# Kernel optimization log

Hardware: AMD Instinct MI355X
Metric: run time of the kernel (lower is better)

The kernel has to match this reference:

```python
import jax, jax.numpy as jnp
import numpy as np

NA, NW, H = 20000, 100000, 128
DA, DW = 64, 128
E_CR, E_IN, E_CO = 400000, 600000, 300000


def _seg_softmax(logits, seg, n):
    m = jax.ops.segment_max(logits, seg, num_segments=n)
    e = jnp.exp(logits - m[seg])
    s = jax.ops.segment_sum(e, seg, num_segments=n)
    return e / (s[seg] + 1e-16)


def _gat(x_src, x_dst, edge, W, b, a_s, a_d):
    # PyG GATConv, heads=1, concat=False, shared lin for src/dst, add_self_loops=True
    n_src, n_dst = x_src.shape[0], x_dst.shape[0]
    loops = jnp.arange(min(n_src, n_dst), dtype=edge.dtype)
    src = jnp.concatenate([edge[0], loops])
    dst = jnp.concatenate([edge[1], loops])
    hs = x_src @ W            # [n_src, H]
    hd = x_dst @ W            # [n_dst, H]
    logit = jax.nn.leaky_relu((hs @ a_s)[src] + (hd @ a_d)[dst], 0.2)
    alpha = _seg_softmax(logit, dst, n_dst)          # softmax over in-neighborhoods
    out = jax.ops.segment_sum(alpha[:, None] * hs[src], dst, num_segments=n_dst)
    return out + b


def _mlp2(x, w1, b1, w2, b2):
    return jax.nn.relu(x @ w1 + b1) @ w2 + b2


def setup_inputs() -> dict:
    key = jax.random.key(0)
    ks = iter(jax.random.split(key, 40))

    def p(shape, scale=0.1):
        return jax.random.normal(next(ks), shape, jnp.float32) * scale

    def edges(n_src, n_dst, E):
        s = jax.random.randint(next(ks), (E,), 0, n_src, dtype=jnp.int32)
        d = jax.random.randint(next(ks), (E,), 0, n_dst, dtype=jnp.int32)
        d = jnp.where(s == d, (d + 1) % n_dst, d)  # keep input loop-free (PyG strips them)
        return jnp.stack([s, d])

    e_creates = edges(NA, NW, E_CR)
    inp = {
        'artist_feat': jax.random.normal(next(ks), (NA, DA), jnp.float32),
        'work_feat': jax.random.normal(next(ks), (NW, DW), jnp.float32),
        'a_w1': p((DA, H)), 'a_b1': jnp.zeros(H, jnp.float32),
        'a_w2': p((H, H)), 'a_b2': jnp.zeros(H, jnp.float32),
        'w_w1': p((DW, H)), 'w_b1': jnp.zeros(H, jnp.float32),
        'w_w2': p((H, H)), 'w_b2': jnp.zeros(H, jnp.float32),
        'cr_W': p((H, H)), 'cr_b': jnp.zeros(H, jnp.float32), 'cr_as': p((H,)), 'cr_ad': p((H,)),
        'in_W': p((H, H)), 'in_b': jnp.zeros(H, jnp.float32), 'in_as': p((H,)), 'in_ad': p((H,)),
        'co_W': p((H, H)), 'co_b': jnp.zeros(H, jnp.float32), 'co_as': p((H,)), 'co_ad': p((H,)),
        'p_w1': p((2 * H, 256)), 'p_b1': jnp.zeros(256, jnp.float32),
        'p_w2': p((256, 128)), 'p_b2': jnp.zeros(128, jnp.float32),
        'p_w3': p((128, 1)), 'p_b3': jnp.zeros(1, jnp.float32),
        'e_creates': e_creates,
        'e_created_by': jnp.flip(e_creates, axis=0),  # reverse relation [work, artist]
        'e_infl': edges(NW, NW, E_IN),
        'e_collab': edges(NA, NA, E_CO),
    }
    return inp


def reference(artist_feat, work_feat,
              a_w1, a_b1, a_w2, a_b2,
              w_w1, w_b1, w_w2, w_b2,
              cr_W, cr_b, cr_as, cr_ad,
              in_W, in_b, in_as, in_ad,
              co_W, co_b, co_as, co_ad,
              p_w1, p_b1, p_w2, p_b2, p_w3, p_b3,
              e_creates, e_created_by, e_infl, e_collab):
    ax = _mlp2(artist_feat, a_w1, a_b1, a_w2, a_b2)      # [NA, H]
    wx = _mlp2(work_feat, w_w1, w_b1, w_w2, w_b2)        # [NW, H]
    wx = jax.nn.elu(_gat(ax, wx, e_creates, cr_W, cr_b, cr_as, cr_ad))
    wx = jax.nn.elu(_gat(wx, wx, e_infl, in_W, in_b, in_as, in_ad))
    au = _gat(wx, ax, e_created_by, cr_W, cr_b, cr_as, cr_ad)  # no elu (matches source)
    ac = jax.nn.elu(_gat(au, au, e_collab, co_W, co_b, co_as, co_ad))
    comb = jnp.concatenate([au, ac], axis=1)             # [NA, 2H]
    h = jax.nn.relu(comb @ p_w1 + p_b1)                  # dropout is identity in eval
    h = jax.nn.relu(h @ p_w2 + p_b2)
    return (h @ p_w3 + p_b3).squeeze()
```

## Files before the change

### kernel.cpp

```cpp
#include <hip/hip_runtime.h>
#include <hip/hip_bf16.h>
#include <cstddef>

#define NA 20000
#define NW 100000
#define HH 128
#define DA 64
#define E_CR 400000
#define E_IN 600000
#define E_CO 300000

#define ROW1 0
#define ROW2 (NW)
#define ROW3 (2 * NW)
#define ROW4 (2 * NW + NA)
#define NTOT (2 * NW + 2 * NA)
#define CAPW 40
#define CAPA 88
#define GNB ((NA + 127) / 128)
#define NPREPG (7 * 128)

typedef short v8s __attribute__((ext_vector_type(8)));
typedef float v4f __attribute__((ext_vector_type(4)));

constexpr int PSLOT = 2 * 128 * 264;

__device__ inline short f2bf(float x) {
    union { float f; unsigned u; } c; c.f = x;
    unsigned r = c.u + 0x7fff + ((c.u >> 16) & 1);
    return (short)(r >> 16);
}
__device__ inline float bf2f(short s) {
    union { unsigned u; float f; } c; c.u = ((unsigned)(unsigned short)s) << 16;
    return c.f;
}
__device__ inline float bfu2f(unsigned short s) {
    union { unsigned u; float f; } c; c.u = ((unsigned)s) << 16;
    return c.f;
}

__device__ inline void split8(const float* xv, v8s& h, v8s& l) {
#pragma unroll
    for (int p = 0; p < 4; ++p) {
        float2 xf; xf.x = xv[2 * p]; xf.y = xv[2 * p + 1];
        __hip_bfloat162 hb = __float22bfloat162_rn(xf);
        float2 hf = __bfloat1622float2(hb);
        float2 lf; lf.x = xf.x - hf.x; lf.y = xf.y - hf.y;
        __hip_bfloat162 lb = __float22bfloat162_rn(lf);
        union { __hip_bfloat162 b; short2 s; } uh, ul;
        uh.b = hb; ul.b = lb;
        h[2 * p] = uh.s.x; h[2 * p + 1] = uh.s.y;
        l[2 * p] = ul.s.x; l[2 * p + 1] = ul.s.y;
    }
}

struct AppChunk { const int* e; int E; int* pad; int cap; int* deg; };

__device__ inline void do_append(const AppChunk& ap, int bid) {
    int b0 = bid * 1024 + threadIdx.x;
    int s[4], d[4]; bool ok[4];
#pragma unroll
    for (int u = 0; u < 4; ++u) {
        int i = b0 + u * 256;
        ok[u] = i < ap.E;
        s[u] = 0; d[u] = 0;
        if (ok[u]) { s[u] = ap.e[i]; d[u] = ap.e[ap.E + i]; }
    }
    int p[4];
#pragma unroll
    for (int u = 0; u < 4; ++u) if (ok[u]) p[u] = atomicAdd(&ap.deg[d[u]], 1);
#pragma unroll
    for (int u = 0; u < 4; ++u)
        if (ok[u] && p[u] < ap.cap)
            ap.pad[(size_t)d[u] * ap.cap + p[u]] = s[u];
}

struct PrepDesc { const float* src; int ldw; int K; };
struct PrepArgs {
    PrepDesc d[10];
    const float *wvW, *wvA;
    const float *ww2, *aw2, *wb2, *ab2;
    float *uW, *u3, *cons, *bf;
    short* wf;
    const float* gX; const float* gB; float* gY; int gM;
};

__global__ __launch_bounds__(256) void k_prep_append(PrepArgs a, short* __restrict__ out,
        AppChunk ap1, AppChunk ap2, AppChunk ap3, AppChunk ap4)
{
    __shared__ short Bs2[2 * 128 * 72];
    int bx = blockIdx.x;

    if (bx == 0) {
        __shared__ float sv[HH];
        int t = threadIdx.x;
        if (t < HH) {
            float s = 0.f;
            for (int j = 0; j < HH; ++j) s += a.wvW[(size_t)t * HH + j] * a.wvA[j];
            sv[t] = s;
        }
        __syncthreads();
        if (t < HH) {
            float s = 0.f;
            for (int j = 0; j < HH; ++j) s += a.ww2[(size_t)t * HH + j] * sv[j];
            a.uW[t] = s;
        } else {
            int k = t - HH;
            float s = 0.f;
            for (int j = 0; j < HH; ++j) s += a.aw2[(size_t)k * HH + j] * sv[j];
            a.u3[k] = s;
        }
        if (t == 0) {
            float s = 0.f;
            for (int j = 0; j < HH; ++j) s += a.wb2[j] * sv[j];
            a.cons[0] = s;
        }
        if (t == 1) {
            float s = 0.f;
            for (int j = 0; j < HH; ++j) s += a.ab2[j] * sv[j];
            a.cons[1] = s;
        }
        return;
    }
    bx -= 1;
    if (bx < 4) {
        int k = bx * 32 + (threadIdx.x >> 3);
        int cb = (threadIdx.x & 7) * 16;
        for (int c = cb; c < cb + 16; ++c) {
            float s = 0.f;
            for (int j = 0; j < HH; ++j) s += a.aw2[(size_t)k * HH + j] * a.wvW[(size_t)j * HH + c];
            short h = f2bf(s);
            short l = f2bf(s - bf2f(h));
            a.wf[c * 136 + k] = h;
            a.wf[128 * 136 + c * 136 + k] = l;
        }
        if (bx == 0 && threadIdx.x < HH) {
            int c = threadIdx.x;
            float s = 0.f;
            for (int j = 0; j < HH; ++j) s += a.ab2[j] * a.wvW[(size_t)j * HH + c];
            a.bf[c] = s;
        }
        return;
    }
    bx -= 4;
    {
        int n1 = (ap1.E + 1023) >> 10;
        if (bx < n1) { do_append(ap1, bx); return; }
        bx -= n1;
        int n2 = (ap2.E + 1023) >> 10;
        if (bx < n2) { do_append(ap2, bx); return; }
        bx -= n2;
        int n3 = (ap3.E + 1023) >> 10;
        if (bx < n3) { do_append(ap3, bx); return; }
        bx -= n3;
        int n4 = (ap4.E + 1023) >> 10;
        if (bx < n4) { do_append(ap4, bx); return; }
        bx -= n4;
    }
    if (bx < GNB) {
        const int bid = bx;
        const int tid = threadIdx.x;
        const int wave = tid >> 6, lane = tid & 63;
        const int l15 = lane & 15, quad = lane >> 4;
        const int wrow = bid * 128 + wave * 32;
        for (int e = tid; e < 64 * 128; e += 256) {
            int n = e & 127, k = e >> 7;
            float x = a.d[0].src[(size_t)k * 128 + n];
            short h = f2bf(x);
            short l = f2bf(x - bf2f(h));
            Bs2[n * 72 + k] = h;
            Bs2[128 * 72 + n * 72 + k] = l;
        }
        v8s ah[2][2], al[2][2];
#pragma unroll
        for (int rf = 0; rf < 2; ++rf) {
            int r = wrow + rf * 16 + l15; if (r >= a.gM) r = a.gM - 1;
            const float* xp = a.gX + (size_t)r * DA + quad * 8;
#pragma unroll
            for (int kf = 0; kf < 2; ++kf) {
                float xv[8];
                *(float4*)&xv[0] = *(const float4*)(xp + kf * 32);
                *(float4*)&xv[4] = *(const float4*)(xp + kf * 32 + 4);
                split8(xv, ah[rf][kf], al[rf][kf]);
            }
        }
        __syncthreads();
        v4f acc[2][8];
#pragma unroll
        for (int rf = 0; rf < 2; ++rf)
#pragma unroll
            for (int cf = 0; cf < 8; ++cf) acc[rf][cf] = (v4f){0.f, 0.f, 0.f, 0.f};
#pragma unroll
        for (int kf = 0; kf < 2; ++kf) {
#pragma unroll
            for (int cf = 0; cf < 8; ++cf) {
                int coff = (cf * 16 + l15) * 72 + kf * 32 + quad * 8;
                v8s bh = *(const v8s*)&Bs2[coff];
                v8s bl = *(const v8s*)&Bs2[128 * 72 + coff];
#pragma unroll
                for (int rf = 0; rf < 2; ++rf) {
                    acc[rf][cf] = __builtin_amdgcn_mfma_f32_16x16x32_bf16(al[rf][kf], bh, acc[rf][cf], 0, 0, 0);
                    acc[rf][cf] = __builtin_amdgcn_mfma_f32_16x16x32_bf16(ah[rf][kf], bl, acc[rf][cf], 0, 0, 0);
                    acc[rf][cf] = __builtin_amdgcn_mfma_f32_16x16x32_bf16(ah[rf][kf], bh, acc[rf][cf], 0, 0, 0);
                }
            }
        }
        float bv[8];
#pragma unroll
        for (int cf = 0; cf < 8; ++cf) bv[cf] = a.gB[cf * 16 + l15];
#pragma unroll
        for (int rf = 0; rf < 2; ++rf) {
#pragma unroll
            for (int reg = 0; reg < 4; ++reg) {
                int r = wrow + rf * 16 + quad * 4 + reg;
                if (r >= a.gM) continue;
                float* yp = a.gY + (size_t)r * HH;
#pragma unroll
                for (int cf = 0; cf < 8; ++cf) {
                    float o = acc[rf][cf][reg] + bv[cf];
                    yp[cf * 16 + l15] = o > 0.f ? o : 0.f;
                }
            }
        }
        return;
    }
    bx -= GNB;
    constexpr int smap[7] = {2, 4, 5, 6, 7, 8, 9};
    int m = smap[bx >> 7];
    int e = (bx & 127) * 256 + threadIdx.x;
    PrepDesc dd = a.d[m];
    int K = dd.K;
    int KP = (K <= 128) ? K + 8 : K;
    if (e >= K * 128) return;
    int n = e & 127, k = e >> 7;
    float x = dd.src[(size_t)k * dd.ldw + n];
    short h = f2bf(x);
    short l = f2bf(x - bf2f(h));
    short* base = out + (size_t)m * PSLOT;
    base[n * KP + k] = h;
    base[128 * KP + n * KP + k] = l;
}

template<int K, int ACT, int NSS, int ST, int LDSB, int OBF, int DUAL, int XBF>
__global__ __launch_bounds__(256, 4) void k_mfma(
    const float* __restrict__ X, int ldx,
    const short* __restrict__ Wp,
    const float* __restrict__ bias,
    float* __restrict__ Y, int ldy, int M,
    const float* __restrict__ v1, float* __restrict__ ss1,
    const float* __restrict__ v2, float* __restrict__ ss2,
    const float* __restrict__ sb)
{
    constexpr int KF = K / 32;
    constexpr int KP = (K <= 128) ? K + 8 : K;
    __shared__ short Bs[LDSB ? 2 * 128 * KP : 8];
    const int tid = threadIdx.x;
    const int wave = tid >> 6, lane = tid & 63;
    const int l15 = lane & 15, quad = lane >> 4;
    int bid = blockIdx.x;
    if (DUAL) {
        int g0 = gridDim.x >> 1;
        if (bid >= g0) { bid -= g0; Wp += PSLOT; bias += 128; Y += 128; }
    }
    const int wrow = bid * 128 + wave * 32;

    if (LDSB) {
        const float4* src = (const float4*)Wp;
        float4* dst = (float4*)Bs;
        constexpr int total = 2 * 128 * KP / 8;
        for (int i = tid; i < total; i += 256) dst[i] = src[i];
        __syncthreads();
    }

    v4f acc[2][8];
#pragma unroll
    for (int rf = 0; rf < 2; ++rf)
#pragma unroll
        for (int cf = 0; cf < 8; ++cf) acc[rf][cf] = (v4f){0.f, 0.f, 0.f, 0.f};

    const unsigned short* xb16[2];
    const float* xb32[2];
#pragma unroll
    for (int rf = 0; rf < 2; ++rf) {
        int r = wrow + rf * 16 + l15; if (r >= M) r = M - 1;
        xb16[rf] = (const unsigned short*)X + (size_t)r * ldx + quad * 8;
        xb32[rf] = X + (size_t)r * ldx + quad * 8;
    }

#pragma unroll
    for (int kf = 0; kf < KF; ++kf) {
        v8s ah[2], al[2];
#pragma unroll
        for (int rf = 0; rf < 2; ++rf) {
            if (XBF) {
                ah[rf] = *(const v8s*)(xb16[rf] + kf * 32);
            } else {
                float xv[8];
                *(float4*)&xv[0] = *(const float4*)(xb32[rf] + kf * 32);
                *(float4*)&xv[4] = *(const float4*)(xb32[rf] + kf * 32 + 4);
                split8(xv, ah[rf], al[rf]);
            }
        }
#pragma unroll
        for (int cf = 0; cf < 8; ++cf) {
            const short* bp = LDSB ? &Bs[(cf * 16 + l15) * KP + kf * 32 + quad * 8]
                                   : Wp + (size_t)(cf * 16 + l15) * KP + kf * 32 + quad * 8;
            v8s bh = *(const v8s*)bp;
            v8s bl = *(const v8s*)(bp + 128 * KP);
#pragma unroll
            for (int rf = 0; rf < 2; ++rf) {
                if (!XBF) acc[rf][cf] = __builtin_amdgcn_mfma_f32_16x16x32_bf16(al[rf], bh, acc[rf][cf], 0, 0, 0);
                acc[rf][cf] = __builtin_amdgcn_mfma_f32_16x16x32_bf16(ah[rf], bl, acc[rf][cf], 0, 0, 0);
                acc[rf][cf] = __builtin_amdgcn_mfma_f32_16x16x32_bf16(ah[rf], bh, acc[rf][cf], 0, 0, 0);
            }
        }
    }

    float bv[8], v1c[8], v2c[8];
#pragma unroll
    for (int cf = 0; cf < 8; ++cf) {
        int col = cf * 16 + l15;
        bv[cf] = bias ? bias[col] : 0.f;
        if (NSS >= 1) v1c[cf] = v1[col];
        if (NSS >= 2) v2c[cf] = v2[col];
    }
    float sbv = (NSS >= 1 && sb) ? sb[0] : 0.f;

#pragma unroll
    for (int rf = 0; rf < 2; ++rf) {
#pragma unroll
        for (int reg = 0; reg < 4; ++reg) {
            int r = wrow + rf * 16 + quad * 4 + reg;
            if (r >= M) continue;
            float p1 = 0.f, p2 = 0.f;
#pragma unroll
            for (int cf = 0; cf < 8; ++cf) {
                float o = acc[rf][cf][reg] + bv[cf];
                if (ACT == 1) o = o > 0.f ? o : 0.f;
                if (NSS >= 1) p1 = fmaf(o, v1c[cf], p1);
                if (NSS >= 2) p2 = fmaf(o, v2c[cf], p2);
                if (ST) {
                    if (OBF) ((unsigned short*)Y)[(size_t)r * ldy + cf * 16 + l15] = (unsigned short)f2bf(o);
                    else     Y[(size_t)r * ldy + cf * 16 + l15] = o;
                }
            }
            if (NSS >= 1) {
#pragma unroll
                for (int w = 1; w < 16; w <<= 1) {
                    p1 += __shfl_xor(p1, w, 64);
                    if (NSS >= 2) p2 += __shfl_xor(p2, w, 64);
                }
                if (l15 == 0) {
                    ss1[r] = p1 + sbv;
                    if (NSS >= 2) ss2[r] = p2;
                }
            }
        }
    }
}

struct MfmaCfg {
    const float* X; int ldx;
    const short* Wp;
    const float* bias;
    float* Y; int ldy; int M;
    int act, nss, obf, xbf, st;
    const float* v1; float* ss1;
    const float* v2; float* ss2;
    const float* sb1;
    const float* vx; float* ssx; const float* cx;
    int nblocks;
};

__global__ __launch_bounds__(256, 4) void k_mfma2(MfmaCfg c0, MfmaCfg c1)
{
    constexpr int KF = 4, KP = 136;
    int bid = blockIdx.x;
    const bool first = bid < c0.nblocks;
    const MfmaCfg& c = first ? c0 : c1;
    if (!first) bid -= c0.nblocks;
    const int tid = threadIdx.x;
    const int wave = tid >> 6, lane = tid & 63;
    const int l15 = lane & 15, quad = lane >> 4;
    const int wrow = bid * 128 + wave * 32;

    v4f acc[2][8];
#pragma unroll
    for (int rf = 0; rf < 2; ++rf)
#pragma unroll
        for (int cf = 0; cf < 8; ++cf) acc[rf][cf] = (v4f){0.f, 0.f, 0.f, 0.f};

    const unsigned short* xb16[2];
    const float* xb32[2];
#pragma unroll
    for (int rf = 0; rf < 2; ++rf) {
        int r = wrow + rf * 16 + l15; if (r >= c.M) r = c.M - 1;
        xb16[rf] = (const unsigned short*)c.X + (size_t)r * c.ldx + quad * 8;
        xb32[rf] = c.X + (size_t)r * c.ldx + quad * 8;
    }

    float px[2] = {0.f, 0.f};
#pragma unroll
    for (int kf = 0; kf < KF; ++kf) {
        v8s ah[2], al[2];
        float uv[8];
        if (c.vx) {
            *(float4*)&uv[0] = *(const float4*)(c.vx + kf * 32 + quad * 8);
            *(float4*)&uv[4] = *(const float4*)(c.vx + kf * 32 + quad * 8 + 4);
        }
#pragma unroll
        for (int rf = 0; rf < 2; ++rf) {
            if (c.xbf) {
                ah[rf] = *(const v8s*)(xb16[rf] + kf * 32);
                al[rf] = (v8s)(short)0;
            } else {
                float xv[8];
                *(float4*)&xv[0] = *(const float4*)(xb32[rf] + kf * 32);
                *(float4*)&xv[4] = *(const float4*)(xb32[rf] + kf * 32 + 4);
                split8(xv, ah[rf], al[rf]);
                if (c.vx) {
#pragma unroll
                    for (int j = 0; j < 8; ++j) px[rf] = fmaf(xv[j], uv[j], px[rf]);
                }
            }
        }
#pragma unroll
        for (int cf = 0; cf < 8; ++cf) {
            const short* bp = c.Wp + (size_t)(cf * 16 + l15) * KP + kf * 32 + quad * 8;
            v8s bh = *(const v8s*)bp;
            v8s bl = *(const v8s*)(bp + 128 * KP);
#pragma unroll
            for (int rf = 0; rf < 2; ++rf) {
                if (!c.xbf) acc[rf][cf] = __builtin_amdgcn_mfma_f32_16x16x32_bf16(al[rf], bh, acc[rf][cf], 0, 0, 0);
                acc[rf][cf] = __builtin_amdgcn_mfma_f32_16x16x32_bf16(ah[rf], bl, acc[rf][cf], 0, 0, 0);
                acc[rf][cf] = __builtin_amdgcn_mfma_f32_16x16x32_bf16(ah[rf], bh, acc[rf][cf], 0, 0, 0);
            }
        }
    }

    if (c.vx) {
        float cxv = c.cx ? c.cx[0] : 0.f;
#pragma unroll
        for (int rf = 0; rf < 2; ++rf) {
            float p = px[rf];
            p += __shfl_xor(p, 16, 64);
            p += __shfl_xor(p, 32, 64);
            int rr = wrow + rf * 16 + l15;
            if (quad == 0 && rr < c.M) c.ssx[rr] = p + cxv;
        }
    }

    float bv[8], v1c[8], v2c[8];
#pragma unroll
    for (int cf = 0; cf < 8; ++cf) {
        int col = cf * 16 + l15;
        bv[cf] = c.bias ? c.bias[col] : 0.f;
        v1c[cf] = (c.nss >= 1) ? c.v1[col] : 0.f;
        v2c[cf] = (c.nss >= 2) ? c.v2[col] : 0.f;
    }
    float sbv = (c.nss >= 1 && c.sb1) ? c.sb1[0] : 0.f;

#pragma unroll
    for (int rf = 0; rf < 2; ++rf) {
#pragma unroll
        for (int reg = 0; reg < 4; ++reg) {
            int r = wrow + rf * 16 + quad * 4 + reg;
            if (r >= c.M) continue;
            float p1 = 0.f, p2 = 0.f;
#pragma unroll
            for (int cf = 0; cf < 8; ++cf) {
                float o = acc[rf][cf][reg] + bv[cf];
                if (c.act) o = o > 0.f ? o : 0.f;
                p1 = fmaf(o, v1c[cf], p1);
                p2 = fmaf(o, v2c[cf], p2);
                if (c.st) {
                    if (c.obf) ((unsigned short*)c.Y)[(size_t)r * c.ldy + cf * 16 + l15] = (unsigned short)f2bf(o);
                    else       c.Y[(size_t)r * c.ldy + cf * 16 + l15] = o;
                }
            }
            if (c.nss >= 1) {
#pragma unroll
                for (int w = 1; w < 16; w <<= 1) {
                    p1 += __shfl_xor(p1, w, 64);
                    p2 += __shfl_xor(p2, w, 64);
                }
                if (l15 == 0) {
                    c.ss1[r] = p1 + sbv;
                    if (c.nss >= 2) c.ss2[r] = p2;
                }
            }
        }
    }
}

template<int ELU, int U, int CAP, int OBF>
__global__ __launch_bounds__(256) void k_aggregate(
    const int* __restrict__ deg, const int* __restrict__ esp,
    const unsigned short* __restrict__ hs, const float* __restrict__ ss,
    const float* __restrict__ sd, const float* __restrict__ bias,
    void* __restrict__ out, int ldy, int n, int loopn)
{
    int lane = threadIdx.x & 63;
    int wv = threadIdx.x >> 6;
    int d = blockIdx.x * 4 + wv;
    if (d >= n) return;
    int half = lane >> 5;
    int col = (lane & 31) * 4;
    const int* row = esp + (size_t)d * CAP;
    int i1 = deg[d]; if (i1 > CAP) i1 = CAP;
    float sdv = sd[d];
    float den = 0.f;
    float ax = 0.f, ay = 0.f, az = 0.f, aw = 0.f;
    if (half == 0 && d < loopn) {
        ushort4 h = *(const ushort4*)(hs + (size_t)d * HH + col);
        float l = ss[d] + sdv;
        l = l < 0.f ? 0.2f * l : l;
        float e = __expf(l);
        den += e;
        ax = fmaf(e, bfu2f(h.x), ax);
        ay = fmaf(e, bfu2f(h.y), ay);
        az = fmaf(e, bfu2f(h.z), az);
        aw = fmaf(e, bfu2f(h.w), aw);
    }
    int i = 0;
    for (; i + 2 * U <= i1; i += 2 * U) {
        int s[U]; ushort4 h[U]; float sv[U];
#pragma unroll
        for (int u = 0; u < U; ++u) s[u] = row[i + 2 * u + half];
#pragma unroll
        for (int u = 0; u < U; ++u) h[u] = *(const ushort4*)(hs + (size_t)s[u] * HH + col);
#pragma unroll
        for (int u = 0; u < U; ++u) sv[u] = ss[s[u]];
#pragma unroll
        for (int u = 0; u < U; ++u) {
            float l = sv[u] + sdv;
            l = l < 0.f ? 0.2f * l : l;
            float e = __expf(l);
            den += e;
            ax = fmaf(e, bfu2f(h[u].x), ax);
            ay = fmaf(e, bfu2f(h[u].y), ay);
            az = fmaf(e, bfu2f(h[u].z), az);
            aw = fmaf(e, bfu2f(h[u].w), aw);
        }
    }
    if (i < i1) {
        int s[U]; ushort4 h[U]; float sv[U]; bool act[U];
#pragma unroll
        for (int u = 0; u < U; ++u) {
            int idx = i + 2 * u + half;
            act[u] = idx < i1;
            s[u] = row[act[u] ? idx : (i1 - 1)];
        }
#pragma unroll
        for (int u = 0; u < U; ++u) h[u] = *(const ushort4*)(hs + (size_t)s[u] * HH + col);
#pragma unroll
        for (int u = 0; u < U; ++u) sv[u] = ss[s[u]];
#pragma unroll
        for (int u = 0; u < U; ++u) {
            float l = sv[u] + sdv;
            l = l < 0.f ? 0.2f * l : l;
            float e = act[u] ? __expf(l) : 0.f;
            den += e;
            ax = fmaf(e, bfu2f(h[u].x), ax);
            ay = fmaf(e, bfu2f(h[u].y), ay);
            az = fmaf(e, bfu2f(h[u].z), az);
            aw = fmaf(e, bfu2f(h[u].w), aw);
        }
    }
    den += __shfl_xor(den, 32, 64);
    ax += __shfl_xor(ax, 32, 64);
    ay += __shfl_xor(ay, 32, 64);
    az += __shfl_xor(az, 32, 64);
    aw += __shfl_xor(aw, 32, 64);
    if (half == 0) {
        float4 b = *(const float4*)(bias + col);
        float inv = 1.f / (den + 1e-16f);
        float o0 = ax * inv + b.x;
        float o1 = ay * inv + b.y;
        float o2 = az * inv + b.z;
        float o3 = aw * inv + b.w;
        if (ELU) {
            o0 = o0 > 0.f ? o0 : expm1f(o0);
            o1 = o1 > 0.f ? o1 : expm1f(o1);
            o2 = o2 > 0.f ? o2 : expm1f(o2);
            o3 = o3 > 0.f ? o3 : expm1f(o3);
        }
        if (OBF) {
            ushort4 ob;
            ob.x = (unsigned short)f2bf(o0);
            ob.y = (unsigned short)f2bf(o1);
            ob.z = (unsigned short)f2bf(o2);
            ob.w = (unsigned short)f2bf(o3);
            *(ushort4*)((unsigned short*)out + (size_t)d * ldy + col) = ob;
        } else {
            *(float4*)((float*)out + (size_t)d * ldy + col) = make_float4(o0, o1, o2, o3);
        }
    }
}

extern "C" void kernel_launch(void* const* d_in, const int* in_sizes, int n_in,
                              void* d_out, int out_size, void* d_ws, size_t ws_size,
                              hipStream_t stream)
{
    const float* artist = (const float*)d_in[0];
    const float* workf  = (const float*)d_in[1];
    const float* a_w1 = (const float*)d_in[2];  const float* a_b1 = (const float*)d_in[3];
    const float* a_w2 = (const float*)d_in[4];  const float* a_b2 = (const float*)d_in[5];
    const float* w_w1 = (const float*)d_in[6];  const float* w_b1 = (const float*)d_in[7];
    const float* w_w2 = (const float*)d_in[8];  const float* w_b2 = (const float*)d_in[9];
    const float* cr_W = (const float*)d_in[10]; const float* cr_b = (const float*)d_in[11];
    const float* cr_as = (const float*)d_in[12]; const float* cr_ad = (const float*)d_in[13];
    const float* in_W = (const float*)d_in[14]; const float* in_b = (const float*)d_in[15];
    const float* in_as = (const float*)d_in[16]; const float* in_ad = (const float*)d_in[17];
    const float* co_W = (const float*)d_in[18]; const float* co_b = (const float*)d_in[19];
    const float* co_as = (const float*)d_in[20]; const float* co_ad = (const float*)d_in[21];
    const float* p_w1 = (const float*)d_in[22]; const float* p_b1 = (const float*)d_in[23];
    const float* p_w2 = (const float*)d_in[24]; const float* p_b2 = (const float*)d_in[25];
    const float* p_w3 = (const float*)d_in[26]; const float* p_b3 = (const float*)d_in[27];
    const int* e_cr = (const int*)d_in[28];
    const int* e_cb = (const int*)d_in[29];
    const int* e_in = (const int*)d_in[30];
    const int* e_co = (const int*)d_in[31];

    char* wsp = (char*)d_ws;
    size_t off = 0;
    auto alloc = [&](size_t bytes) -> void* {
        void* p = wsp + off;
        off += (bytes + 255) / 256 * 256;
        return p;
    };
    float* hsA  = (float*)alloc((size_t)NA * HH * 4);
    unsigned short* wxb = (unsigned short*)alloc((size_t)NW * HH * 2);
    unsigned short* hsb = (unsigned short*)alloc((size_t)NW * HH * 2);
    float* h1   = (float*)alloc((size_t)NA * 256 * 4);
    float* comb = (float*)alloc((size_t)NA * 256 * 4);
    float* ss1 = (float*)alloc((size_t)NA * 4);
    float* sd1 = (float*)alloc((size_t)NW * 4);
    float* ss2 = (float*)alloc((size_t)NW * 4);
    float* sd2 = (float*)alloc((size_t)NW * 4);
    float* ss3 = (float*)alloc((size_t)NW * 4);
    float* sd3 = (float*)alloc((size_t)NA * 4);
    float* ss4 = (float*)alloc((size_t)NA * 4);
    float* sd4 = (float*)alloc((size_t)NA * 4);
    float* uW  = (float*)alloc(HH * 4);
    float* u3v = (float*)alloc(HH * 4);
    float* bfv = (float*)alloc(HH * 4);
    float* cons = (float*)alloc(2 * 4);
    int* deg   = (int*)alloc((size_t)NTOT * 4);
    int* pad1  = (int*)alloc((size_t)NW * CAPW * 4);
    int* pad2  = (int*)alloc((size_t)NW * CAPW * 4);
    int* pad3  = (int*)alloc((size_t)NA * CAPA * 4);
    int* pad4  = (int*)alloc((size_t)NA * CAPA * 4);
    short* preW = (short*)alloc((size_t)10 * PSLOT * 2);
    (void)ws_size; (void)in_sizes; (void)n_in; (void)out_size;

    auto pre = [&](int m) { return preW + (size_t)m * PSLOT; };
    auto gg = [](int M) { return (M + 127) / 128; };
    auto apb = [](int E) { return (E + 1023) / 1024; };
    const float* nf = nullptr;
    float* nfm = nullptr;

    PrepArgs pa;
    pa.d[0] = {a_w1, HH, DA};
    pa.d[1] = {a_w2, HH, HH};
    pa.d[2] = {w_w1, HH, HH};
    pa.d[3] = {w_w2, HH, HH};
    pa.d[4] = {cr_W, HH, HH};
    pa.d[5] = {in_W, HH, HH};
    pa.d[6] = {co_W, HH, HH};
    pa.d[7] = {p_w1, 256, 256};
    pa.d[8] = {p_w1 + 128, 256, 256};
    pa.d[9] = {p_w2, HH, 256};
    pa.wvW = cr_W; pa.wvA = cr_ad;
    pa.ww2 = w_w2; pa.aw2 = a_w2; pa.wb2 = w_b2; pa.ab2 = a_b2;
    pa.uW = uW; pa.u3 = u3v; pa.cons = cons; pa.bf = bfv;
    pa.wf = pre(1);
    pa.gX = artist; pa.gB = a_b1; pa.gY = hsA; pa.gM = NA;

    AppChunk ap1 = {e_cr, E_CR, pad1, CAPW, deg + ROW1};
    AppChunk ap2 = {e_in, E_IN, pad2, CAPW, deg + ROW2};
    AppChunk ap3 = {e_cb, E_CR, pad3, CAPA, deg + ROW3};
    AppChunk ap4 = {e_co, E_CO, pad4, CAPA, deg + ROW4};

    (void)hipMemsetAsync(deg, 0, (size_t)NTOT * 4, stream);

    {
        int nblk = 5 + apb(E_CR) + apb(E_IN) + apb(E_CR) + apb(E_CO) + GNB + NPREPG;
        k_prep_append<<<nblk, 256, 0, stream>>>(pa, preW, ap1, ap2, ap3, ap4);
    }

    {
        MfmaCfg c0 = {workf, HH, pre(2), w_b1, nullptr, HH, NW,
                      1, 1, 0, 0, 0,
                      uW, sd1, nf, nfm,
                      cons,
                      nf, nfm, nf,
                      gg(NW)};
        MfmaCfg c1 = {hsA, HH, pre(1), bfv, (float*)hsb, HH, NA,
                      0, 1, 1, 0, 1,
                      cr_as, ss1, nf, nfm,
                      nf,
                      u3v, sd3, cons + 1,
                      gg(NA)};
        k_mfma2<<<gg(NW) + gg(NA), 256, 0, stream>>>(c0, c1);
    }

    k_aggregate<1, 2, CAPW, 1><<<(NW + 3) / 4, 256, 0, stream>>>(deg + ROW1, pad1, hsb, ss1, sd1, cr_b, wxb, HH, NW, NA);

    k_mfma<HH, 0, 2, 1, 0, 1, 0, 1><<<gg(NW), 256, 0, stream>>>((const float*)wxb, HH, pre(5), nullptr, (float*)hsb, HH, NW, in_as, ss2, in_ad, sd2, nf);
    k_aggregate<1, 2, CAPW, 1><<<(NW + 3) / 4, 256, 0, stream>>>(deg + ROW2, pad2, hsb, ss2, sd2, in_b, wxb, HH, NW, NW);

    k_mfma<HH, 0, 1, 1, 0, 1, 0, 1><<<gg(NW), 256, 0, stream>>>((const float*)wxb, HH, pre(4), nullptr, (float*)hsb, HH, NW, cr_as, ss3, nf, nfm, nf);
    k_aggregate<0, 4, CAPA, 0><<<(NA + 3) / 4, 256, 0, stream>>>(deg + ROW3, pad3, hsb, ss3, sd3, cr_b, comb, 256, NA, NA);

    k_mfma<HH, 0, 2, 1, 0, 1, 0, 0><<<gg(NA), 256, 0, stream>>>(comb, 256, pre(6), nullptr, (float*)hsb, HH, NA, co_as, ss4, co_ad, sd4, nf);
    k_aggregate<1, 4, CAPA, 0><<<(NA + 3) / 4, 256, 0, stream>>>(deg + ROW4, pad4, hsb, ss4, sd4, co_b, comb + 128, 256, NA, NA);

    k_mfma<256, 1, 0, 1, 0, 0, 1, 0><<<2 * gg(NA), 256, 0, stream>>>(comb, 256, pre(7), p_b1, h1, 256, NA, nf, nfm, nf, nfm, nf);
    k_mfma<256, 1, 1, 0, 0, 0, 0, 0><<<gg(NA), 256, 0, stream>>>(h1, 256, pre(9), p_b2, nfm, 0, NA, p_w3, (float*)d_out, nf, nfm, p_b3);
}
```

Baseline: 705.0 us.

## Spread edge-append passes across later MFMA kernels to overlap with GEMMs

```diff
diff --git a/kernel.cpp b/kernel.cpp
--- a/kernel.cpp
+++ b/kernel.cpp
@@ -86,7 +86,7 @@
 };
 
 __global__ __launch_bounds__(256) void k_prep_append(PrepArgs a, short* __restrict__ out,
-        AppChunk ap1, AppChunk ap2, AppChunk ap3, AppChunk ap4)
+                                                     AppChunk ap)
 {
     __shared__ short Bs2[2 * 128 * 72];
     int bx = blockIdx.x;
@@ -144,18 +144,9 @@
     }
     bx -= 4;
     {
-        int n1 = (ap1.E + 1023) >> 10;
-        if (bx < n1) { do_append(ap1, bx); return; }
+        int n1 = (ap.E + 1023) >> 10;
+        if (bx < n1) { do_append(ap, bx); return; }
         bx -= n1;
-        int n2 = (ap2.E + 1023) >> 10;
-        if (bx < n2) { do_append(ap2, bx); return; }
-        bx -= n2;
-        int n3 = (ap3.E + 1023) >> 10;
-        if (bx < n3) { do_append(ap3, bx); return; }
-        bx -= n3;
-        int n4 = (ap4.E + 1023) >> 10;
-        if (bx < n4) { do_append(ap4, bx); return; }
-        bx -= n4;
     }
     if (bx < GNB) {
         const int bid = bx;
@@ -372,10 +363,13 @@
     int nblocks;
 };
 
-__global__ __launch_bounds__(256, 4) void k_mfma2(MfmaCfg c0, MfmaCfg c1)
+__global__ __launch_bounds__(256, 4) void k_mfma2(MfmaCfg c0, MfmaCfg c1, AppChunk ap)
 {
     constexpr int KF = 4, KP = 136;
+    const int napp = (ap.E + 1023) >> 10;
     int bid = blockIdx.x;
+    if (bid < napp) { do_append(ap, bid); return; }
+    bid -= napp;
     const bool first = bid < c0.nblocks;
     const MfmaCfg& c = first ? c0 : c1;
     if (!first) bid -= c0.nblocks;
@@ -681,12 +675,13 @@
     AppChunk ap2 = {e_in, E_IN, pad2, CAPW, deg + ROW2};
     AppChunk ap3 = {e_cb, E_CR, pad3, CAPA, deg + ROW3};
     AppChunk ap4 = {e_co, E_CO, pad4, CAPA, deg + ROW4};
+    AppChunk ap0 = {nullptr, 0, nullptr, 1, nullptr};
 
     (void)hipMemsetAsync(deg, 0, (size_t)NTOT * 4, stream);
 
     {
-        int nblk = 5 + apb(E_CR) + apb(E_IN) + apb(E_CR) + apb(E_CO) + GNB + NPREPG;
-        k_prep_append<<<nblk, 256, 0, stream>>>(pa, preW, ap1, ap2, ap3, ap4);
+        int nblk = 5 + apb(E_CR) + GNB + NPREPG;
+        k_prep_append<<<nblk, 256, 0, stream>>>(pa, preW, ap1);
     }
 
     {
@@ -702,15 +697,31 @@
                       nf,
                       u3v, sd3, cons + 1,
                       gg(NA)};
-        k_mfma2<<<gg(NW) + gg(NA), 256, 0, stream>>>(c0, c1);
+        k_mfma2<<<apb(E_IN) + gg(NW) + gg(NA), 256, 0, stream>>>(c0, c1, ap2);
     }
 
     k_aggregate<1, 2, CAPW, 1><<<(NW + 3) / 4, 256, 0, stream>>>(deg + ROW1, pad1, hsb, ss1, sd1, cr_b, wxb, HH, NW, NA);
 
-    k_mfma<HH, 0, 2, 1, 0, 1, 0, 1><<<gg(NW), 256, 0, stream>>>((const float*)wxb, HH, pre(5), nullptr, (float*)hsb, HH, NW, in_as, ss2, in_ad, sd2, nf);
+    {
+        MfmaCfg c0 = {(const float*)wxb, HH, pre(5), nullptr, (float*)hsb, HH, NW,
+                      0, 2, 1, 1, 1,
+                      in_as, ss2, in_ad, sd2,
+                      nf, nf, nfm, nf,
+                      gg(NW)};
+        MfmaCfg c1 = c0; c1.nblocks = 0;
+        k_mfma2<<<apb(E_CR) + gg(NW), 256, 0, stream>>>(c0, c1, ap3);
+    }
     k_aggregate<1, 2, CAPW, 1><<<(NW + 3) / 4, 256, 0, stream>>>(deg + ROW2, pad2, hsb, ss2, sd2, in_b, wxb, HH, NW, NW);
 
-    k_mfma<HH, 0, 1, 1, 0, 1, 0, 1><<<gg(NW), 256, 0, stream>>>((const float*)wxb, HH, pre(4), nullptr, (float*)hsb, HH, NW, cr_as, ss3, nf, nfm, nf);
+    {
+        MfmaCfg c0 = {(const float*)wxb, HH, pre(4), nullptr, (float*)hsb, HH, NW,
+                      0, 1, 1, 1, 1,
+                      cr_as, ss3, nf, nfm,
+                      nf, nf, nfm, nf,
+                      gg(NW)};
+        MfmaCfg c1 = c0; c1.nblocks = 0;
+        k_mfma2<<<apb(E_CO) + gg(NW), 256, 0, stream>>>(c0, c1, ap4);
+    }
     k_aggregate<0, 4, CAPA, 0><<<(NA + 3) / 4, 256, 0, stream>>>(deg + ROW3, pad3, hsb, ss3, sd3, cr_b, comb, 256, NA, NA);
 
     k_mfma<HH, 0, 2, 1, 0, 1, 0, 0><<<gg(NA), 256, 0, stream>>>(comb, 256, pre(6), nullptr, (float*)hsb, HH, NA, co_as, ss4, co_ad, sd4, nf);
@@ -718,4 +729,5 @@
 
     k_mfma<256, 1, 0, 1, 0, 0, 1, 0><<<2 * gg(NA), 256, 0, stream>>>(comb, 256, pre(7), p_b1, h1, 256, NA, nf, nfm, nf, nfm, nf);
     k_mfma<256, 1, 1, 0, 0, 0, 0, 0><<<gg(NA), 256, 0, stream>>>(h1, 256, pre(9), p_b2, nfm, 0, NA, p_w3, (float*)d_out, nf, nfm, p_b3);
-}
+    (void)ap0;
+}
```

Result: faster. 683.0 us (-3.1%).
